# Optimization experiments

Hardware: AMD Instinct MI355X
Metric: run time of the kernel (lower is better)

Reference implementation:

```python
import jax, jax.numpy as jnp
import numpy as np

B, C, N, K = 8, 192, 3136, 9
OUT_CH = 192
BN_EPS = 1e-5


def setup_inputs() -> dict:
    key = jax.random.key(0)
    k1, k2, k3, k4 = jax.random.split(key, 4)
    x = jax.random.normal(k1, (B, C, N, 1), dtype=jnp.float32)
    y = jax.random.normal(k2, (B, C, N, 1), dtype=jnp.float32)
    edge_index = jax.random.randint(k3, (2, B, N, K), 0, N, dtype=jnp.int64)
    # 1x1 conv weight (out_ch, in_ch*2), no bias (BatchNorm follows)
    W = jax.random.normal(k4, (OUT_CH, 2 * C), dtype=jnp.float32) / np.sqrt(2 * C)
    gamma = jnp.ones((OUT_CH,), dtype=jnp.float32)
    beta = jnp.zeros((OUT_CH,), dtype=jnp.float32)
    return {"x": x, "y": y, "edge_index": edge_index, "W": W, "gamma": gamma, "beta": beta}


def _gather(feat, idx):
    # feat: (B, C, N); idx: (B, M, K) -> (B, C, M, K)
    return jax.vmap(lambda f, i: f[:, i])(feat, idx)


def reference(x, y, edge_index, W, gamma, beta):
    xt = x[..., 0]  # (B, C, N)
    yt = y[..., 0]
    x_i = _gather(xt, edge_index[1])          # (B, C, N, K)
    x_j = _gather(yt, edge_index[0])          # (B, C, N, K)
    rel = jnp.max(x_j - x_i, axis=-1, keepdims=True)  # (B, C, N, 1)
    h = jnp.concatenate([x, rel], axis=1)     # (B, 2C, N, 1)
    # 1x1 conv
    out = jnp.einsum('oc,bcnk->bonk', W, h)   # (B, out_ch, N, 1)
    # BatchNorm2d (training-mode batch statistics)
    mean = out.mean(axis=(0, 2, 3), keepdims=True)
    var = out.var(axis=(0, 2, 3), keepdims=True)
    out = (out - mean) * jax.lax.rsqrt(var + BN_EPS)
    out = out * gamma[None, :, None, None] + beta[None, :, None, None]
    return jax.nn.gelu(out, approximate=False)
```

## Files before the change

### kernel.cpp

```cpp
#include <hip/hip_runtime.h>
#include <hip/hip_bf16.h>

#define B_    8
#define C_    192
#define N_    3136
#define K_    9
#define OC    192
#define KDIM  384
#define ROWS  (B_ * N_)
#define BNK   (B_ * N_ * K_)

typedef __hip_bfloat16 bf16;
using short8 = __attribute__((ext_vector_type(8))) short;
using us4    = __attribute__((ext_vector_type(4))) unsigned short;
using f32x4  = __attribute__((ext_vector_type(4))) float;

__device__ inline float bfbits2f(unsigned short u) {
    unsigned int x = ((unsigned int)u) << 16;
    return __builtin_bit_cast(float, x);
}
__device__ inline bf16 f2bf(float v) { return __float2bfloat16(v); }
__device__ inline unsigned short f2bfbits(float v) {
    bf16 t = __float2bfloat16(v);
    return *reinterpret_cast<unsigned short*>(&t);
}

__global__ void k_prep(const float* __restrict__ x, const float* __restrict__ y,
                       const float* __restrict__ W,
                       bf16* __restrict__ h, bf16* __restrict__ yT,
                       bf16* __restrict__ Wb, float* __restrict__ stats) {
    int tx = threadIdx.x, ty = threadIdx.y;
    int bz = blockIdx.z;
    if (bz == 16) {
        int flat = blockIdx.y * 98 + blockIdx.x;
        int t = ty * 32 + tx;
        if (flat < 288) {
            int i = flat * 256 + t;
            Wb[i] = f2bf(W[i]);
        }
        if (flat == 0) stats[t] = 0.f;
        if (flat == 1 && t < 128) stats[256 + t] = 0.f;
        return;
    }
    __shared__ float tile[32][33];
    int n0 = blockIdx.x * 32, c0 = blockIdx.y * 32;
    int b = bz >> 1, which = bz & 1;
    const float* src = which ? y : x;
#pragma unroll
    for (int i = 0; i < 4; i++) {
        int c = c0 + ty + i * 8;
        tile[ty + i * 8][tx] = src[((size_t)b * C_ + c) * N_ + n0 + tx];
    }
    __syncthreads();
    if (which == 0) {
#pragma unroll
        for (int i = 0; i < 4; i++) {
            int n = n0 + ty + i * 8;
            h[((size_t)b * N_ + n) * KDIM + c0 + tx] = f2bf(tile[tx][ty + i * 8]);
        }
    } else {
#pragma unroll
        for (int i = 0; i < 4; i++) {
            int n = n0 + ty + i * 8;
            yT[((size_t)b * N_ + n) * C_ + c0 + tx] = f2bf(tile[tx][ty + i * 8]);
        }
    }
}

__launch_bounds__(256)
__global__ void k_gather_rel(const int* __restrict__ ei, bf16* __restrict__ h,
                             const bf16* __restrict__ yT) {
    const int wave = threadIdx.x >> 6;
    const int lane = threadIdx.x & 63;
    const int b   = blockIdx.x & 7;
    const int n   = (blockIdx.x >> 3) * 4 + wave;
    const int r   = b * N_ + n;

    const int* e0 = ei + (size_t)r * K_;
    const int* e1 = ei + (size_t)BNK + (size_t)r * K_;
    int ej[K_], ex[K_];
#pragma unroll
    for (int k = 0; k < K_; k++) { ej[k] = e0[k]; ex[k] = e1[k]; }

    const us4* y4 = (const us4*)(yT + (size_t)b * N_ * C_);
    const us4* x4 = (const us4*)(h + (size_t)b * N_ * KDIM);

    if (lane < 48) {
        float m0 = -3.4e38f, m1 = -3.4e38f, m2 = -3.4e38f, m3 = -3.4e38f;
#pragma unroll
        for (int k = 0; k < K_; k++) {
            us4 vy = y4[(size_t)ej[k] * 48 + lane];
            us4 vx = x4[(size_t)ex[k] * 96 + lane];
            m0 = fmaxf(m0, bfbits2f(vy.x) - bfbits2f(vx.x));
            m1 = fmaxf(m1, bfbits2f(vy.y) - bfbits2f(vx.y));
            m2 = fmaxf(m2, bfbits2f(vy.z) - bfbits2f(vx.z));
            m3 = fmaxf(m3, bfbits2f(vy.w) - bfbits2f(vx.w));
        }
        us4 o;
        o.x = f2bfbits(m0); o.y = f2bfbits(m1);
        o.z = f2bfbits(m2); o.w = f2bfbits(m3);
        *((us4*)(h + (size_t)r * KDIM + C_) + lane) = o;
    }
}

__launch_bounds__(192)
__global__ void k_gemm_stats(const bf16* __restrict__ h, const bf16* __restrict__ Wb,
                             float* __restrict__ stats) {
    int tid = threadIdx.x;
    int wave = tid >> 6, lane = tid & 63;
    int fcol = lane & 15, fgrp = lane >> 4;
    int r0 = blockIdx.x * 64;
    int colbase = wave * 64;

    f32x4 acc[4][4] = {};

    for (int kk = 0; kk < 12; kk++) {
        short8 a[4], bb[4];
#pragma unroll
        for (int i = 0; i < 4; i++)
            a[i] = *reinterpret_cast<const short8*>(
                h + (size_t)(r0 + i * 16 + fcol) * KDIM + kk * 32 + fgrp * 8);
#pragma unroll
        for (int j = 0; j < 4; j++)
            bb[j] = *reinterpret_cast<const short8*>(
                Wb + (size_t)(colbase + j * 16 + fcol) * KDIM + kk * 32 + fgrp * 8);
#pragma unroll
        for (int i = 0; i < 4; i++)
#pragma unroll
            for (int j = 0; j < 4; j++)
                acc[i][j] = __builtin_amdgcn_mfma_f32_16x16x32_bf16(a[i], bb[j], acc[i][j], 0, 0, 0);
    }

#pragma unroll
    for (int j = 0; j < 4; j++) {
        int o = colbase + j * 16 + fcol;
        float s1 = 0.f, s2 = 0.f;
#pragma unroll
        for (int i = 0; i < 4; i++)
#pragma unroll
            for (int e = 0; e < 4; e++) {
                float v = acc[i][j][e];
                s1 += v;
                s2 += v * v;
            }
        s1 += __shfl_xor(s1, 16); s1 += __shfl_xor(s1, 32);
        s2 += __shfl_xor(s2, 16); s2 += __shfl_xor(s2, 32);
        if (fgrp == 0) {
            atomicAdd(&stats[o], s1);
            atomicAdd(&stats[OC + o], s2);
        }
    }
}

__launch_bounds__(192)
__global__ void k_gemm_bn(const bf16* __restrict__ h, const bf16* __restrict__ Wb,
                          const float* __restrict__ stats,
                          const float* __restrict__ gamma, const float* __restrict__ beta,
                          float* __restrict__ out) {
    int tid = threadIdx.x;
    int wave = tid >> 6, lane = tid & 63;
    int fcol = lane & 15, fgrp = lane >> 4;
    int r0 = blockIdx.x * 64;
    int b = r0 / N_;
    int n0 = r0 % N_;
    int colbase = wave * 64;

    f32x4 acc[4][4] = {};

    for (int kk = 0; kk < 12; kk++) {
        short8 wfr[4], hfr[4];
#pragma unroll
        for (int i = 0; i < 4; i++)
            wfr[i] = *reinterpret_cast<const short8*>(
                Wb + (size_t)(colbase + i * 16 + fcol) * KDIM + kk * 32 + fgrp * 8);
#pragma unroll
        for (int j = 0; j < 4; j++)
            hfr[j] = *reinterpret_cast<const short8*>(
                h + (size_t)(r0 + j * 16 + fcol) * KDIM + kk * 32 + fgrp * 8);
#pragma unroll
        for (int i = 0; i < 4; i++)
#pragma unroll
            for (int j = 0; j < 4; j++)
                acc[i][j] = __builtin_amdgcn_mfma_f32_16x16x32_bf16(wfr[i], hfr[j], acc[i][j], 0, 0, 0);
    }

    const float invc = 1.0f / (float)ROWS;
#pragma unroll
    for (int i = 0; i < 4; i++) {
#pragma unroll
        for (int e = 0; e < 4; e++) {
            int o = colbase + i * 16 + fgrp * 4 + e;
            float mean = stats[o] * invc;
            float var  = stats[OC + o] * invc - mean * mean;
            float is   = rsqrtf(var + 1e-5f);
            float sc = gamma[o] * is;
            float sh = beta[o] - mean * sc;
#pragma unroll
            for (int j = 0; j < 4; j++) {
                float z = acc[i][j][e] * sc + sh;
                float gl = 0.5f * z * (1.0f + erff(z * 0.70710678118654752f));
                out[((size_t)b * OC + o) * N_ + n0 + j * 16 + fcol] = gl;
            }
        }
    }
}

extern "C" void kernel_launch(void* const* d_in, const int* in_sizes, int n_in,
                              void* d_out, int out_size, void* d_ws, size_t ws_size,
                              hipStream_t stream) {
    const float* x     = (const float*)d_in[0];
    const float* y     = (const float*)d_in[1];
    const int*   ei    = (const int*)d_in[2];
    const float* W     = (const float*)d_in[3];
    const float* gamma = (const float*)d_in[4];
    const float* beta  = (const float*)d_in[5];
    float* out = (float*)d_out;

    char* ws = (char*)d_ws;
    bf16*  h     = (bf16*)(ws);
    bf16*  yT    = (bf16*)(ws + 19267584);
    bf16*  Wb    = (bf16*)(ws + 19267584 + 9633792);
    float* stats = (float*)(ws + 19267584 + 9633792 + 147456);

    dim3 bt(32, 8);
    k_prep<<<dim3(N_ / 32, C_ / 32, 2 * B_ + 1), bt, 0, stream>>>(x, y, W, h, yT, Wb, stats);
    k_gather_rel<<<ROWS / 4, 256, 0, stream>>>(ei, h, yT);
    k_gemm_stats<<<ROWS / 64, 192, 0, stream>>>(h, Wb, stats);
    k_gemm_bn<<<ROWS / 64, 192, 0, stream>>>(h, Wb, stats, gamma, beta, out);
}
```

Before: 165.8 us.

## Store GEMM output once and apply BN+GELU in separate transpose kernel

Instead of recomputing the 1x1-conv GEMM in a second pass after batch statistics are known, the first GEMM now writes its fp32 result to a workspace buffer while accumulating stats. A new tiled transpose kernel reads that buffer, applies batch-norm and exact GELU, and writes the channel-major output. This removes the duplicated MFMA work and the second read of h. In exchange it adds a full fp32 intermediate write and read, plus strided stores in the GEMM epilogue.

Result: faster. 149.4 us (-9.9%).

```diff
diff --git a/kernel.cpp b/kernel.cpp
--- a/kernel.cpp
+++ b/kernel.cpp
@@ -104,8 +104,8 @@
 }
 
 __launch_bounds__(192)
-__global__ void k_gemm_stats(const bf16* __restrict__ h, const bf16* __restrict__ Wb,
-                             float* __restrict__ stats) {
+__global__ void k_gemm(const bf16* __restrict__ h, const bf16* __restrict__ Wb,
+                       float* __restrict__ outp, float* __restrict__ stats) {
     int tid = threadIdx.x;
     int wave = tid >> 6, lane = tid & 63;
     int fcol = lane & 15, fgrp = lane >> 4;
@@ -136,13 +136,16 @@
         int o = colbase + j * 16 + fcol;
         float s1 = 0.f, s2 = 0.f;
 #pragma unroll
-        for (int i = 0; i < 4; i++)
+        for (int i = 0; i < 4; i++) {
+            int rbase = r0 + i * 16 + fgrp * 4;
 #pragma unroll
             for (int e = 0; e < 4; e++) {
                 float v = acc[i][j][e];
+                outp[(size_t)(rbase + e) * OC + o] = v;
                 s1 += v;
                 s2 += v * v;
             }
+        }
         s1 += __shfl_xor(s1, 16); s1 += __shfl_xor(s1, 32);
         s2 += __shfl_xor(s2, 16); s2 += __shfl_xor(s2, 32);
         if (fgrp == 0) {
@@ -152,56 +155,30 @@
     }
 }
 
-__launch_bounds__(192)
-__global__ void k_gemm_bn(const bf16* __restrict__ h, const bf16* __restrict__ Wb,
-                          const float* __restrict__ stats,
+__global__ void k_bn_gelu(const float* __restrict__ outp, const float* __restrict__ stats,
                           const float* __restrict__ gamma, const float* __restrict__ beta,
                           float* __restrict__ out) {
-    int tid = threadIdx.x;
-    int wave = tid >> 6, lane = tid & 63;
-    int fcol = lane & 15, fgrp = lane >> 4;
-    int r0 = blockIdx.x * 64;
-    int b = r0 / N_;
-    int n0 = r0 % N_;
-    int colbase = wave * 64;
-
-    f32x4 acc[4][4] = {};
-
-    for (int kk = 0; kk < 12; kk++) {
-        short8 wfr[4], hfr[4];
-#pragma unroll
-        for (int i = 0; i < 4; i++)
-            wfr[i] = *reinterpret_cast<const short8*>(
-                Wb + (size_t)(colbase + i * 16 + fcol) * KDIM + kk * 32 + fgrp * 8);
-#pragma unroll
-        for (int j = 0; j < 4; j++)
-            hfr[j] = *reinterpret_cast<const short8*>(
-                h + (size_t)(r0 + j * 16 + fcol) * KDIM + kk * 32 + fgrp * 8);
-#pragma unroll
-        for (int i = 0; i < 4; i++)
-#pragma unroll
-            for (int j = 0; j < 4; j++)
-                acc[i][j] = __builtin_amdgcn_mfma_f32_16x16x32_bf16(wfr[i], hfr[j], acc[i][j], 0, 0, 0);
-    }
-
+    __shared__ float tile[32][33];
+    int tx = threadIdx.x, ty = threadIdx.y;
+    int n0 = blockIdx.x * 32, o0 = blockIdx.y * 32, b = blockIdx.z;
+#pragma unroll
+    for (int i = 0; i < 4; i++) {
+        int n = n0 + ty + i * 8;
+        tile[ty + i * 8][tx] = outp[(size_t)(b * N_ + n) * OC + o0 + tx];
+    }
+    __syncthreads();
     const float invc = 1.0f / (float)ROWS;
 #pragma unroll
     for (int i = 0; i < 4; i++) {
-#pragma unroll
-        for (int e = 0; e < 4; e++) {
-            int o = colbase + i * 16 + fgrp * 4 + e;
-            float mean = stats[o] * invc;
-            float var  = stats[OC + o] * invc - mean * mean;
-            float is   = rsqrtf(var + 1e-5f);
-            float sc = gamma[o] * is;
-            float sh = beta[o] - mean * sc;
-#pragma unroll
-            for (int j = 0; j < 4; j++) {
-                float z = acc[i][j][e] * sc + sh;
-                float gl = 0.5f * z * (1.0f + erff(z * 0.70710678118654752f));
-                out[((size_t)b * OC + o) * N_ + n0 + j * 16 + fcol] = gl;
-            }
-        }
+        int o = o0 + ty + i * 8;
+        float mean = stats[o] * invc;
+        float var  = stats[OC + o] * invc - mean * mean;
+        float is   = rsqrtf(var + 1e-5f);
+        float g = gamma[o], bt = beta[o];
+        float v = tile[tx][ty + i * 8];
+        float z = (v - mean) * is * g + bt;
+        float gl = 0.5f * z * (1.0f + erff(z * 0.70710678118654752f));
+        out[((size_t)b * OC + o) * N_ + n0 + tx] = gl;
     }
 }
 
@@ -219,12 +196,13 @@
     char* ws = (char*)d_ws;
     bf16*  h     = (bf16*)(ws);
     bf16*  yT    = (bf16*)(ws + 19267584);
-    bf16*  Wb    = (bf16*)(ws + 19267584 + 9633792);
-    float* stats = (float*)(ws + 19267584 + 9633792 + 147456);
+    bf16*  Wb    = (bf16*)(ws + 28901376);
+    float* stats = (float*)(ws + 29048832);
+    float* outp  = (float*)(ws + 29050368);
 
     dim3 bt(32, 8);
     k_prep<<<dim3(N_ / 32, C_ / 32, 2 * B_ + 1), bt, 0, stream>>>(x, y, W, h, yT, Wb, stats);
     k_gather_rel<<<ROWS / 4, 256, 0, stream>>>(ei, h, yT);
-    k_gemm_stats<<<ROWS / 64, 192, 0, stream>>>(h, Wb, stats);
-    k_gemm_bn<<<ROWS / 64, 192, 0, stream>>>(h, Wb, stats, gamma, beta, out);
-}
+    k_gemm<<<ROWS / 64, 192, 0, stream>>>(h, Wb, outp, stats);
+    k_bn_gelu<<<dim3(N_ / 32, OC / 32, B_), bt, 0, stream>>>(outp, stats, gamma, beta, out);
+}
```
